# Kernel tuning notes

Hardware: AMD Instinct MI355X
Metric: run time of the kernel (lower is better)

Reference implementation:

```python
import jax, jax.numpy as jnp
import numpy as np

B = 1048576
D = 48
D3 = ((D - 1) // 3 + 1) * 3  # 48
NB = D3 // 3                 # 16 blocks


def setup_inputs() -> dict:
    key = jax.random.key(0)
    k1, k2, k3, k4, k5 = jax.random.split(key, 5)
    rho_real = jax.random.normal(k1, (B, 2, 2), dtype=jnp.float32)
    rho_imag = jax.random.normal(k2, (B, 2, 2), dtype=jnp.float32)
    x = jax.random.normal(k3, (B, D), dtype=jnp.float32)
    w = jax.random.normal(k4, (D,), dtype=jnp.float32) * np.float32(np.sqrt(2.0 / 3.0))
    theta = jax.random.normal(k5, (D3,), dtype=jnp.float32) * np.float32(0.1)
    return {"rho_real": rho_real, "rho_imag": rho_imag, "x": x, "w": w, "theta": theta}


def _apply_blocks(rho, phi):
    # phi: [B, D3]; rho: [B, 2, 2] complex64
    phi_blocks = phi.reshape(phi.shape[0], NB, 3).transpose(1, 0, 2)  # [NB, B, 3]

    def step(r, p):
        a = p[:, 0] * 0.5                       # rotation half-angle
        b = (p[:, 1] + p[:, 2]) * 0.5           # sum phase
        c = (p[:, 1] - p[:, 2]) * 0.5           # diff phase
        ca, sa = jnp.cos(a), jnp.sin(a)
        eb = jnp.exp(1j * b)                    # complex64
        ec = jnp.exp(1j * c)
        row0 = jnp.stack([ca * eb, -sa * ec], axis=-1)
        row1 = jnp.stack([sa * jnp.conj(ec), ca * jnp.conj(eb)], axis=-1)
        U = jnp.stack([row0, row1], axis=-2)    # [B, 2, 2]
        r = jnp.einsum('bim,bmn,bjn->bij', U, r, jnp.conj(U))
        return r, None

    rho, _ = jax.lax.scan(step, rho, phi_blocks)
    return rho


def reference(rho_real, rho_imag, x, w, theta):
    rho = (rho_real + 1j * rho_imag).astype(jnp.complex64)  # [B,2,2]
    wx = x * w                                              # einsum 'j,bj->bj'
    phi = theta[None, :] + jnp.pad(wx, ((0, 0), (0, D3 - D)))
    return _apply_blocks(rho, phi)
```

## Files before the change

kernel.cpp:

```cpp
#include <hip/hip_runtime.h>

#define BLK 256
#define DD  48
#define STR 257

__global__ __launch_bounds__(BLK) void qlayer_kernel(
    const float* __restrict__ rho_real,
    const float* __restrict__ rho_imag,
    const float* __restrict__ x,
    const float* __restrict__ w,
    const float* __restrict__ theta,
    float* __restrict__ out,
    long long n,
    long long out_floats)
{
    __shared__ float sx[24 * STR];

    const int tid = threadIdx.x;
    const long long blockBase = (long long)blockIdx.x * BLK;
    const long long b = blockBase + tid;
    const bool active = (b < n);

    float a0r = 0.f, v1r = 0.f, v1i = 0.f, v2r = 0.f, v2i = 0.f, v3r = 0.f, v3i = 0.f;
    if (active) {
        float4 rr = reinterpret_cast<const float4*>(rho_real)[b];
        float4 ri = reinterpret_cast<const float4*>(rho_imag)[b];
        a0r = 0.5f * (rr.x + rr.w);
        v1r = 0.5f * (rr.y + rr.z);  v1i = 0.5f * (ri.y + ri.z);
        v2r = 0.5f * (ri.z - ri.y);  v2i = 0.5f * (rr.y - rr.z);
        v3r = 0.5f * (rr.x - rr.w);  v3i = 0.5f * (ri.x - ri.w);
    }

    const float4* __restrict__ x4 = reinterpret_cast<const float4*>(x);

    #pragma unroll
    for (int h = 0; h < 2; ++h) {
        #pragma unroll
        for (int i = 0; i < 6; ++i) {
            int f = tid + BLK * i;
            int e = f / 6;
            int q = f - 6 * e;
            long long ge = blockBase + e;
            float4 v = make_float4(0.f, 0.f, 0.f, 0.f);
            if (ge < n) v = x4[ge * 12 + h * 6 + q];
            int jb = q * 4;
            sx[(jb + 0) * STR + e] = v.x;
            sx[(jb + 1) * STR + e] = v.y;
            sx[(jb + 2) * STR + e] = v.z;
            sx[(jb + 3) * STR + e] = v.w;
        }
        __syncthreads();

        #pragma unroll
        for (int r = 0; r < 8; ++r) {
            const int J = 24 * h + 3 * r;
            float p0 = fmaf(sx[(3 * r + 0) * STR + tid], w[J + 0], theta[J + 0]);
            float p1 = fmaf(sx[(3 * r + 1) * STR + tid], w[J + 1], theta[J + 1]);
            float p2 = fmaf(sx[(3 * r + 2) * STR + tid], w[J + 2], theta[J + 2]);

            float s0, c0, s1, c1, s2, c2;
            __sincosf(p0, &s0, &c0);
            __sincosf(p1, &s1, &c1);
            __sincosf(p2, &s2, &c2);

            float n1r = fmaf(c2, v1r,  s2 * v2r);
            float n1i = fmaf(c2, v1i,  s2 * v2i);
            float n2r = fmaf(c2, v2r, -s2 * v1r);
            float n2i = fmaf(c2, v2i, -s2 * v1i);
            float m1r = fmaf(c0, n1r,  s0 * v3r);
            float m1i = fmaf(c0, n1i,  s0 * v3i);
            float m3r = fmaf(c0, v3r, -s0 * n1r);
            float m3i = fmaf(c0, v3i, -s0 * n1i);
            v1r = fmaf(c1, m1r,  s1 * n2r);
            v1i = fmaf(c1, m1i,  s1 * n2i);
            v2r = fmaf(c1, n2r, -s1 * m1r);
            v2i = fmaf(c1, n2i, -s1 * m1i);
            v3r = m3r;
            v3i = m3i;
        }
        if (h == 0) __syncthreads();
    }

    if (active) {
        if (4 * b + 4 <= out_floats) {
            reinterpret_cast<float4*>(out)[b] =
                make_float4(a0r + v3r, v1r + v2i, v1r - v2i, a0r - v3r);
        } else {
            float vals[4] = {a0r + v3r, v1r + v2i, v1r - v2i, a0r - v3r};
            for (int j = 0; j < 4; ++j) {
                long long o = 4 * b + j;
                if (o < out_floats) out[o] = vals[j];
            }
        }
    }
}

extern "C" void kernel_launch(void* const* d_in, const int* in_sizes, int n_in,
                              void* d_out, int out_size, void* d_ws, size_t ws_size,
                              hipStream_t stream) {
    const float* rho_real = (const float*)d_in[0];
    const float* rho_imag = (const float*)d_in[1];
    const float* x        = (const float*)d_in[2];
    const float* w        = (const float*)d_in[3];
    const float* theta    = (const float*)d_in[4];
    float* out = (float*)d_out;

    long long nB = (long long)in_sizes[0] / 4;
    long long nX = (long long)in_sizes[2] / DD;
    long long n  = nB < nX ? nB : nX;
    if (n <= 0) return;

    int grid = (int)((n + BLK - 1) / BLK);
    qlayer_kernel<<<dim3(grid), dim3(BLK), 0, stream>>>(
        rho_real, rho_imag, x, w, theta, out, n, (long long)out_size);
}
```

Measured before the change: 323.9 us.

## Merge adjacent Z rotations across blocks and use native revolution-scaled sin/cos

Consecutive Z-axis rotations (the last angle of one block and the second angle of the next) are combined into one rotation by summing their angles. This removes about a third of the sincos evaluations and rotation FMAs per element. The sin/cos calls now use the AMDGCN hardware builtins, which take their input in revolutions, so each angle is pre-scaled by 1/(2π). The angle merge relies on both rotations acting on the same vector pair. The raw hardware sin/cos may lose accuracy for larger arguments.

```diff
diff --git a/kernel.cpp b/kernel.cpp
--- a/kernel.cpp
+++ b/kernel.cpp
@@ -3,6 +3,7 @@
 #define BLK 256
 #define DD  48
 #define STR 257
+#define INV2PI 0.15915494309189535f
 
 __global__ __launch_bounds__(BLK) void qlayer_kernel(
     const float* __restrict__ rho_real,
@@ -33,8 +34,7 @@
 
     const float4* __restrict__ x4 = reinterpret_cast<const float4*>(x);
 
-    #pragma unroll
-    for (int h = 0; h < 2; ++h) {
+    auto stage = [&](int h) {
         #pragma unroll
         for (int i = 0; i < 6; ++i) {
             int f = tid + BLK * i;
@@ -43,43 +43,62 @@
             long long ge = blockBase + e;
             float4 v = make_float4(0.f, 0.f, 0.f, 0.f);
             if (ge < n) v = x4[ge * 12 + h * 6 + q];
-            int jb = q * 4;
+            int jb = 4 * q;
             sx[(jb + 0) * STR + e] = v.x;
             sx[(jb + 1) * STR + e] = v.y;
             sx[(jb + 2) * STR + e] = v.z;
             sx[(jb + 3) * STR + e] = v.w;
         }
-        __syncthreads();
+    };
 
-        #pragma unroll
-        for (int r = 0; r < 8; ++r) {
-            const int J = 24 * h + 3 * r;
-            float p0 = fmaf(sx[(3 * r + 0) * STR + tid], w[J + 0], theta[J + 0]);
-            float p1 = fmaf(sx[(3 * r + 1) * STR + tid], w[J + 1], theta[J + 1]);
-            float p2 = fmaf(sx[(3 * r + 2) * STR + tid], w[J + 2], theta[J + 2]);
+    auto rotZ = [&](float ang) {
+        float s = __builtin_amdgcn_sinf(ang * INV2PI);
+        float c = __builtin_amdgcn_cosf(ang * INV2PI);
+        float t1r = fmaf(c, v1r,  s * v2r);
+        float t1i = fmaf(c, v1i,  s * v2i);
+        v2r = fmaf(c, v2r, -s * v1r);
+        v2i = fmaf(c, v2i, -s * v1i);
+        v1r = t1r; v1i = t1i;
+    };
+    auto rotY = [&](float ang) {
+        float s = __builtin_amdgcn_sinf(ang * INV2PI);
+        float c = __builtin_amdgcn_cosf(ang * INV2PI);
+        float t1r = fmaf(c, v1r,  s * v3r);
+        float t1i = fmaf(c, v1i,  s * v3i);
+        v3r = fmaf(c, v3r, -s * v1r);
+        v3i = fmaf(c, v3i, -s * v1i);
+        v1r = t1r; v1i = t1i;
+    };
+    auto xl = [&](int row) { return sx[row * STR + tid]; };
 
-            float s0, c0, s1, c1, s2, c2;
-            __sincosf(p0, &s0, &c0);
-            __sincosf(p1, &s1, &c1);
-            __sincosf(p2, &s2, &c2);
+    stage(0);
+    __syncthreads();
 
-            float n1r = fmaf(c2, v1r,  s2 * v2r);
-            float n1i = fmaf(c2, v1i,  s2 * v2i);
-            float n2r = fmaf(c2, v2r, -s2 * v1r);
-            float n2i = fmaf(c2, v2i, -s2 * v1i);
-            float m1r = fmaf(c0, n1r,  s0 * v3r);
-            float m1i = fmaf(c0, n1i,  s0 * v3i);
-            float m3r = fmaf(c0, v3r, -s0 * n1r);
-            float m3i = fmaf(c0, v3i, -s0 * n1i);
-            v1r = fmaf(c1, m1r,  s1 * n2r);
-            v1i = fmaf(c1, m1i,  s1 * n2i);
-            v2r = fmaf(c1, n2r, -s1 * m1r);
-            v2i = fmaf(c1, n2i, -s1 * m1i);
-            v3r = m3r;
-            v3i = m3i;
-        }
-        if (h == 0) __syncthreads();
+    rotZ(fmaf(xl(2), w[2], theta[2]));
+    #pragma unroll
+    for (int k = 0; k < 7; ++k) {
+        const int j = 3 * k;
+        rotY(fmaf(xl(j), w[j], theta[j]));
+        float ts = theta[j + 1] + theta[j + 5];
+        rotZ(fmaf(xl(j + 1), w[j + 1], fmaf(xl(j + 5), w[j + 5], ts)));
     }
+    rotY(fmaf(xl(21), w[21], theta[21]));
+    float x22 = xl(22);
+    __syncthreads();
+
+    stage(1);
+    __syncthreads();
+
+    rotZ(fmaf(x22, w[22], fmaf(xl(26 - 24), w[26], theta[22] + theta[26])));
+    #pragma unroll
+    for (int k = 8; k < 15; ++k) {
+        const int j = 3 * k;
+        rotY(fmaf(xl(j - 24), w[j], theta[j]));
+        float ts = theta[j + 1] + theta[j + 5];
+        rotZ(fmaf(xl(j - 23), w[j + 1], fmaf(xl(j - 19), w[j + 5], ts)));
+    }
+    rotY(fmaf(xl(45 - 24), w[45], theta[45]));
+    rotZ(fmaf(xl(46 - 24), w[46], theta[46]));
 
     if (active) {
         if (4 * b + 4 <= out_floats) {
```

Result: no change. 321.1 us (-0.8%).
